# Optimization experiments

Measured on AMD Instinct MI355X. Metric: run time of the kernel, lower is better.

## Reference

```python
import jax, jax.numpy as jnp
import numpy as np


def _gru(x, w_ih, w_hh, b_ih, b_hh, reverse=False):
    # PyTorch GRU cell math. x: (N, T, Din) -> (N, T, Hh)
    N, T, _ = x.shape
    Hh = w_hh.shape[1]
    xp = jnp.einsum('ntd,gd->ntg', x, w_ih) + b_ih  # (N, T, 3*Hh), input gates precomputed

    def step(h, xp_t):
        gh = h @ w_hh.T + b_hh
        ir, iz, inn = jnp.split(xp_t, 3, axis=-1)
        hr, hz, hn = jnp.split(gh, 3, axis=-1)
        r = jax.nn.sigmoid(ir + hr)
        z = jax.nn.sigmoid(iz + hz)
        n = jnp.tanh(inn + r * hn)
        h_new = (1.0 - z) * n + z * h
        return h_new, h_new

    h0 = jnp.zeros((N, Hh), x.dtype)
    _, ys = jax.lax.scan(step, h0, jnp.swapaxes(xp, 0, 1), reverse=reverse)
    return jnp.swapaxes(ys, 0, 1)


def _bigru(x, pf, pb):
    return jnp.concatenate([_gru(x, *pf), _gru(x, *pb, reverse=True)], axis=-1)


def _attn(out, w, b, ctx):
    # out: (N, T, H). tanh(Linear) -> context dot -> softmax -> weighted sum
    u = jnp.tanh(jnp.einsum('nth,gh->ntg', out, w) + b)
    a = jax.nn.softmax(u @ ctx, axis=-1)  # (N, T)
    return jnp.einsum('nt,nth->nh', a, out)


def setup_inputs() -> dict:
    key = jax.random.key(0)
    H, Hh = 512, 256
    S, B, Nsent = 2048, 16, 16
    L = S // Nsent
    ks = jax.random.split(key, 32)

    def p(k, shape):
        return jax.random.normal(k, shape, jnp.float32) * 0.05

    starts = jnp.arange(Nsent, dtype=jnp.int32) * L
    spans = jnp.stack([starts, starts + L], axis=-1)  # (Nsent, 2)
    spans = jnp.broadcast_to(spans, (B, Nsent, 2))

    inp = {
        'token_feats': jax.random.normal(ks[0], (S, B, H), jnp.float32),
        'sentence_spans': spans,
        # word BiGRU params (forward / backward directions)
        'w_wih_f': p(ks[1], (3 * Hh, H)), 'w_whh_f': p(ks[2], (3 * Hh, Hh)),
        'w_bih_f': p(ks[3], (3 * Hh,)), 'w_bhh_f': p(ks[4], (3 * Hh,)),
        'w_wih_b': p(ks[5], (3 * Hh, H)), 'w_whh_b': p(ks[6], (3 * Hh, Hh)),
        'w_bih_b': p(ks[7], (3 * Hh,)), 'w_bhh_b': p(ks[8], (3 * Hh,)),
        # sentence BiGRU params
        's_wih_f': p(ks[9], (3 * Hh, H)), 's_whh_f': p(ks[10], (3 * Hh, Hh)),
        's_bih_f': p(ks[11], (3 * Hh,)), 's_bhh_f': p(ks[12], (3 * Hh,)),
        's_wih_b': p(ks[13], (3 * Hh, H)), 's_whh_b': p(ks[14], (3 * Hh, Hh)),
        's_bih_b': p(ks[15], (3 * Hh,)), 's_bhh_b': p(ks[16], (3 * Hh,)),
        # attention params
        'w_attn_w': p(ks[17], (H, H)), 'w_attn_b': p(ks[18], (H,)),
        'w_ctx': jax.random.normal(ks[19], (H,), jnp.float32),
        's_attn_w': p(ks[20], (H, H)), 's_attn_b': p(ks[21], (H,)),
        's_ctx': jax.random.normal(ks[22], (H,), jnp.float32),
    }
    return inp


def reference(token_feats, sentence_spans,
              w_wih_f, w_whh_f, w_bih_f, w_bhh_f,
              w_wih_b, w_whh_b, w_bih_b, w_bhh_b,
              s_wih_f, s_whh_f, s_bih_f, s_bhh_f,
              s_wih_b, s_whh_b, s_bih_b, s_bhh_b,
              w_attn_w, w_attn_b, w_ctx,
              s_attn_w, s_attn_b, s_ctx):
    S, B, H = token_feats.shape
    Nsent = sentence_spans.shape[1]
    L = S // Nsent  # uniform spans: segment b,i = tokens [i*L, (i+1)*L)

    x = jnp.swapaxes(token_feats, 0, 1)  # (B, S, H)
    segs = x.reshape(B * Nsent, L, H)    # all sentences batched together

    # word-level BiGRU + word attention -> sentence vectors
    out_w = _bigru(segs, (w_wih_f, w_whh_f, w_bih_f, w_bhh_f),
                   (w_wih_b, w_whh_b, w_bih_b, w_bhh_b))  # (B*Nsent, L, H)
    sent_vecs = _attn(out_w, w_attn_w, w_attn_b, w_ctx).reshape(B, Nsent, H)

    # sentence-level BiGRU + sentence attention (no padding: all masks true)
    out_s = _bigru(sent_vecs, (s_wih_f, s_whh_f, s_bih_f, s_bhh_f),
                   (s_wih_b, s_whh_b, s_bih_b, s_bhh_b))  # (B, Nsent, H)
    Yh = _attn(out_s, s_attn_w, s_attn_b, s_ctx)  # (B, H)
    return Yh
```

## Files before the change

### kernel.cpp

```cpp
#include <hip/hip_runtime.h>
#include <stdint.h>


using uint32  = unsigned int;
using bf16x8  = __attribute__((ext_vector_type(8))) __bf16;
using floatx4 = __attribute__((ext_vector_type(4))) float;

__device__ __forceinline__ float b2f(unsigned short u) {
    union { uint32 i; float f; } v; v.i = ((uint32)u) << 16; return v.f;
}
__device__ __forceinline__ unsigned short f2b(float f) {
    union { float f; uint32 i; } v; v.f = f;
    uint32 r = v.i + 0x7fffu + ((v.i >> 16) & 1u);
    return (unsigned short)(r >> 16);
}
__device__ __forceinline__ float sigmoidf_(float x) { return 1.f / (1.f + __expf(-x)); }
__device__ __forceinline__ float tanhf_(float x) {
    x = fminf(15.f, fmaxf(-15.f, x));
    float e = __expf(2.f * x);
    return (e - 1.f) / (e + 1.f);
}

__device__ __forceinline__ void gl16(const unsigned short* g, unsigned short* l) {
    __builtin_amdgcn_global_load_lds(
        (const __attribute__((address_space(1))) uint32*)g,
        (__attribute__((address_space(3))) uint32*)l, 16, 0, 0);
}

#define O_XPC     0L
#define O_OWHI    50331648L
#define O_OWLO    83886080L
#define O_STATE   117440512L
#define O_SCW     117964800L
#define O_W0HI    118095872L
#define O_W0LO    118882304L
#define O_W1HI    119668736L
#define O_W1LO    120455168L
#define O_WAHI    121241600L
#define O_WALO    121765888L
#define O_S0HI    122290176L
#define O_S0LO    123076608L
#define O_S1HI    123863040L
#define O_S1LO    124649472L
#define O_SAHI    125435904L
#define O_SALO    125960192L
#define O_HW0     126484480L
#define O_HW1     126877696L
#define O_HS0     127270912L
#define O_HS1     127664128L
#define O_SENTHI  128057344L
#define O_SENTLO  128319488L
#define O_XPS     128581632L
#define O_SSTATE  130154496L
#define O_OSHI    130187264L
#define O_OSLO    130449408L
#define O_SCS     130711552L
#define O_TKWH    130712576L
#define O_TKWL    147489792L

__global__ __launch_bounds__(256)
void cvt_hilo6(const float* __restrict__ s0, const float* __restrict__ s1,
               const float* __restrict__ s2, const float* __restrict__ s3,
               const float* __restrict__ s4, const float* __restrict__ s5,
               char* __restrict__ ws)
{
    const int b = blockIdx.x;
    const float* src; unsigned short *hi, *lo; int base;
    if (b < 192)      { src = s0; hi = (unsigned short*)(ws + O_W0HI); lo = (unsigned short*)(ws + O_W0LO); base = b; }
    else if (b < 384) { src = s1; hi = (unsigned short*)(ws + O_W1HI); lo = (unsigned short*)(ws + O_W1LO); base = b - 192; }
    else if (b < 576) { src = s2; hi = (unsigned short*)(ws + O_S0HI); lo = (unsigned short*)(ws + O_S0LO); base = b - 384; }
    else if (b < 768) { src = s3; hi = (unsigned short*)(ws + O_S1HI); lo = (unsigned short*)(ws + O_S1LO); base = b - 576; }
    else if (b < 896) { src = s4; hi = (unsigned short*)(ws + O_WAHI); lo = (unsigned short*)(ws + O_WALO); base = b - 768; }
    else              { src = s5; hi = (unsigned short*)(ws + O_SAHI); lo = (unsigned short*)(ws + O_SALO); base = b - 896; }
    const int idx = (base * 256 + threadIdx.x) * 8;
    float f[8];
    *reinterpret_cast<float4*>(&f[0]) = *reinterpret_cast<const float4*>(src + idx);
    *reinterpret_cast<float4*>(&f[4]) = *reinterpret_cast<const float4*>(src + idx + 4);
    unsigned short h[8], l[8];
    #pragma unroll
    for (int j = 0; j < 8; ++j) {
        h[j] = f2b(f[j]);
        l[j] = f2b(f[j] - b2f(h[j]));
    }
    *reinterpret_cast<uint4*>(hi + idx) = *reinterpret_cast<const uint4*>(h);
    *reinterpret_cast<uint4*>(lo + idx) = *reinterpret_cast<const uint4*>(l);
}

__global__ __launch_bounds__(256)
void cvt_b4(const float* __restrict__ s0, const float* __restrict__ s1,
            const float* __restrict__ s2, const float* __restrict__ s3,
            char* __restrict__ ws)
{
    const int b = blockIdx.x;
    const float* src; unsigned short* dst; int base;
    if (b < 96)       { src = s0; dst = (unsigned short*)(ws + O_HW0); base = b; }
    else if (b < 192) { src = s1; dst = (unsigned short*)(ws + O_HW1); base = b - 96; }
    else if (b < 288) { src = s2; dst = (unsigned short*)(ws + O_HS0); base = b - 192; }
    else              { src = s3; dst = (unsigned short*)(ws + O_HS1); base = b - 288; }
    const int idx = (base * 256 + threadIdx.x) * 8;
    float f[8];
    *reinterpret_cast<float4*>(&f[0]) = *reinterpret_cast<const float4*>(src + idx);
    *reinterpret_cast<float4*>(&f[4]) = *reinterpret_cast<const float4*>(src + idx + 4);
    unsigned short o[8];
    #pragma unroll
    for (int j = 0; j < 8; ++j) o[j] = f2b(f[j]);
    *reinterpret_cast<uint4*>(dst + idx) = *reinterpret_cast<const uint4*>(o);
}

__global__ __launch_bounds__(256)
void cvt_tokwin(const float* __restrict__ tok, unsigned short* __restrict__ whi,
                unsigned short* __restrict__ wlo, int c32)
{
    const int u = blockIdx.x * 256 + threadIdx.x;
    const int h8 = u & 63;
    const int rest = u >> 6;
    const int w = rest & 63, seq = rest >> 6;
    const int sent = seq & 15, b = seq >> 4;
    const int t = (w < 32) ? (c32 + w) : (96 - c32 + (w - 32));
    const long src = ((long)(sent * 128 + t) * 16 + b) * 512 + h8 * 8;
    float f[8];
    *reinterpret_cast<float4*>(&f[0]) = *reinterpret_cast<const float4*>(tok + src);
    *reinterpret_cast<float4*>(&f[4]) = *reinterpret_cast<const float4*>(tok + src + 4);
    unsigned short h[8], l[8];
    #pragma unroll
    for (int j = 0; j < 8; ++j) {
        h[j] = f2b(f[j]);
        l[j] = f2b(f[j] - b2f(h[j]));
    }
    const long dst = (long)rest * 512 + h8 * 8;
    *reinterpret_cast<uint4*>(whi + dst) = *reinterpret_cast<const uint4*>(h);
    *reinterpret_cast<uint4*>(wlo + dst) = *reinterpret_cast<const uint4*>(l);
}

template<int AMODE>
__device__ __forceinline__ long amap(int m, int t0, int sgn) {
    if (AMODE == 1) {
        const int sq = m >> 5, tl = m & 31;
        return (long)(sq * 64 + t0 + sgn * tl) * 512;
    } else if (AMODE == 3) {
        const int n = m >> 4, tl = m & 15;
        return (long)(n * 16 + t0 + sgn * tl) * 512;
    }
    return (long)m * 512;
}

template<int AMODE, int OUT>
__global__ __launch_bounds__(256)
void gemm_g(const unsigned short* __restrict__ Ahi, const unsigned short* __restrict__ Alo,
            const unsigned short* __restrict__ Wh0, const unsigned short* __restrict__ Wl0,
            const unsigned short* __restrict__ Wh1, const unsigned short* __restrict__ Wl1,
            const float* __restrict__ b0, const float* __restrict__ b1,
            float* __restrict__ C, int ldC, long c1off,
            float* __restrict__ score, const float* __restrict__ ctx,
            int t00, int t01, int nbyHalf)
{
    __shared__ __align__(16) unsigned short smem[16384];
    unsigned short* Ahs = smem;
    unsigned short* Als = smem + 4096;
    unsigned short* Whs = smem + 8192;
    unsigned short* Wls = smem + 12288;

    int bx = blockIdx.x, by = blockIdx.y;
    {
        const int nbx = gridDim.x, nby = gridDim.y;
        if ((nby & 7) == 0) {
            const int l = by * nbx + bx;
            const int xcd = l & 7;
            const int s = l >> 3;
            bx = s % nbx;
            by = xcd * (nby >> 3) + s / nbx;
        }
    }

    const int tid  = threadIdx.x;
    const int lane = tid & 63;
    const int wave = tid >> 6;
    const int wm = wave >> 1, wn = wave & 1;
    const int n_base = bx * 128;
    const int q = lane >> 4;
    const int r = lane & 15;

    const unsigned short* Whi = Wh0;
    const unsigned short* Wlo = Wl0;
    const float* bias = b0;
    float* Cb = C;
    int t0 = t00, sgn = 1, m_base;
    if (nbyHalf > 0 && by >= nbyHalf) {
        Whi = Wh1; Wlo = Wl1; bias = b1; Cb = C + c1off;
        t0 = t01; sgn = -1;
        m_base = (by - nbyHalf) * 128;
    } else {
        m_base = by * 128;
    }

    long aoff[2], woff[2];
    #pragma unroll
    for (int i = 0; i < 2; ++i) {
        const int s = tid + 256 * i;
        const int R = s >> 2, kg = s & 3;
        const int kq = (kg - (R >> 1)) & 3;
        aoff[i] = amap<AMODE>(m_base + R, t0, sgn) + kq * 8;
        woff[i] = (long)(n_base + R) * 512 + kq * 8;
    }

    floatx4 acc[4][4];
    #pragma unroll
    for (int mt = 0; mt < 4; ++mt)
        #pragma unroll
        for (int nt = 0; nt < 4; ++nt) acc[mt][nt] = (floatx4){0.f, 0.f, 0.f, 0.f};

    for (int k0 = 0; k0 < 512; k0 += 32) {
        #pragma unroll
        for (int i = 0; i < 2; ++i) {
            const int ld = tid * 8 + i * 2048;
            gl16(Ahi + aoff[i] + k0, Ahs + ld);
            gl16(Alo + aoff[i] + k0, Als + ld);
            gl16(Whi + woff[i] + k0, Whs + ld);
            gl16(Wlo + woff[i] + k0, Wls + ld);
        }
        __syncthreads();

        bf16x8 ah[4], al[4];
        #pragma unroll
        for (int mt = 0; mt < 4; ++mt) {
            const int R = wm * 64 + mt * 16 + r;
            const int s = R * 4 + ((q + (R >> 1)) & 3);
            ah[mt] = *reinterpret_cast<const bf16x8*>(Ahs + s * 8);
            al[mt] = *reinterpret_cast<const bf16x8*>(Als + s * 8);
        }
        #pragma unroll
        for (int nt = 0; nt < 4; ++nt) {
            const int Rn = wn * 64 + nt * 16 + r;
            const int s = Rn * 4 + ((q + (Rn >> 1)) & 3);
            bf16x8 wh = *reinterpret_cast<const bf16x8*>(Whs + s * 8);
            bf16x8 wl = *reinterpret_cast<const bf16x8*>(Wls + s * 8);
            #pragma unroll
            for (int mt = 0; mt < 4; ++mt) {
                acc[mt][nt] = __builtin_amdgcn_mfma_f32_16x16x32_bf16(ah[mt], wh, acc[mt][nt], 0, 0, 0);
                acc[mt][nt] = __builtin_amdgcn_mfma_f32_16x16x32_bf16(ah[mt], wl, acc[mt][nt], 0, 0, 0);
                acc[mt][nt] = __builtin_amdgcn_mfma_f32_16x16x32_bf16(al[mt], wh, acc[mt][nt], 0, 0, 0);
            }
        }
        __syncthreads();
    }

    if (OUT == 0) {
        #pragma unroll
        for (int nt = 0; nt < 4; ++nt) {
            const int n = n_base + wn * 64 + nt * 16 + r;
            const float bs = bias[n];
            #pragma unroll
            for (int mt = 0; mt < 4; ++mt) {
                const int m = m_base + wm * 64 + mt * 16 + q * 4;
                #pragma unroll
                for (int e = 0; e < 4; ++e)
                    Cb[(long)(m + e) * ldC + n] = acc[mt][nt][e] + bs;
            }
        }
    } else {
        #pragma unroll
        for (int mt = 0; mt < 4; ++mt) {
            float p[4] = {0.f, 0.f, 0.f, 0.f};
            #pragma unroll
            for (int nt = 0; nt < 4; ++nt) {
                const int n = n_base + wn * 64 + nt * 16 + r;
                const float cx = ctx[n];
                const float bs = bias[n];
                #pragma unroll
                for (int e = 0; e < 4; ++e)
                    p[e] += cx * tanhf_(acc[mt][nt][e] + bs);
            }
            #pragma unroll
            for (int mk = 1; mk < 16; mk <<= 1) {
                #pragma unroll
                for (int e = 0; e < 4; ++e) p[e] += __shfl_xor(p[e], mk, 64);
            }
            if (r == 0) {
                const int m = m_base + wm * 64 + mt * 16 + q * 4;
                #pragma unroll
                for (int e = 0; e < 4; ++e)
                    atomicAdd(&score[m + e], p[e]);
            }
        }
    }
}

__global__ __launch_bounds__(512, 2)
void gru2(const float* __restrict__ xp,
          const unsigned short* __restrict__ Wf,
          const unsigned short* __restrict__ Wb,
          const float* __restrict__ bhf, const float* __restrict__ bhb,
          float* __restrict__ state,
          unsigned short* __restrict__ ohi, unsigned short* __restrict__ olo,
          int steps, int t0f, int t0b, int groups, int Tout)
{
    __shared__ float pre[768 * 5];
    __shared__ unsigned short Bf[8 * 64 * 8];

    const int tid  = threadIdx.x;
    const int lane = tid & 63;
    const int w    = tid >> 6;
    const int dir  = blockIdx.x / groups;
    const int g    = blockIdx.x % groups;
    const int nseq = groups * 2;
    const unsigned short* W = dir ? Wb : Wf;
    const float* bh = dir ? bhb : bhf;
    const int t0  = dir ? t0b : t0f;
    const int sgn = dir ? -1 : 1;

    const int s = tid >> 8;
    const int j = tid & 255;
    const float bhr = bh[j], bhz = bh[j + 256], bhn = bh[j + 512];

    bf16x8 wf[6][8];
    {
        const int r0 = w * 96 + (lane & 15);
        const int kf = (lane >> 4) * 8;
        #pragma unroll
        for (int mt = 0; mt < 6; ++mt)
            #pragma unroll
            for (int kk = 0; kk < 8; ++kk)
                wf[mt][kk] = *reinterpret_cast<const bf16x8*>(
                    W + (long)(r0 + mt * 16) * 256 + kk * 32 + kf);
    }

    #pragma unroll
    for (int i = 0; i < 4; ++i)
        reinterpret_cast<uint32*>(Bf)[tid * 4 + i] = 0;

    float h = state[((long)dir * nseq + g * 2 + s) * 256 + j];
    const int posHi = ((j >> 5) * 64 + ((j >> 3) & 3) * 16 + s) * 8 + (j & 7);
    const int posLo = ((j >> 5) * 64 + ((j >> 3) & 3) * 16 + 2 + s) * 8 + (j & 7);
    {
        const unsigned short hb = f2b(h);
        Bf[posHi] = hb;
        Bf[posLo] = f2b(h - b2f(hb));
    }
    __syncthreads();

    const float* xbase = xp + (long)dir * nseq * steps * 768
                       + (long)(g * 2 + s) * steps * 768;
    const int q = lane >> 4, r = lane & 15;

    for (int st = 0; st < steps; ++st) {
        const int t = t0 + sgn * st;

        const float* xb = xbase + (long)st * 768;
        const float xr = xb[j];
        const float xz = xb[256 + j];
        const float xn = xb[512 + j];

        floatx4 acc[6];
        #pragma unroll
        for (int mt = 0; mt < 6; ++mt) acc[mt] = (floatx4){0.f, 0.f, 0.f, 0.f};
        #pragma unroll
        for (int kk = 0; kk < 8; ++kk) {
            bf16x8 bv = *reinterpret_cast<const bf16x8*>(Bf + (kk * 64 + lane) * 8);
            #pragma unroll
            for (int mt = 0; mt < 6; ++mt)
                acc[mt] = __builtin_amdgcn_mfma_f32_16x16x32_bf16(wf[mt][kk], bv, acc[mt], 0, 0, 0);
        }
        if (r < 4) {
            #pragma unroll
            for (int mt = 0; mt < 6; ++mt) {
                const int row = w * 96 + mt * 16 + q * 4;
                #pragma unroll
                for (int e = 0; e < 4; ++e)
                    pre[(row + e) * 5 + r] = acc[mt][e];
            }
        }
        __syncthreads();

        {
            const float pr = pre[j * 5 + s]         + pre[j * 5 + 2 + s];
            const float pz = pre[(j + 256) * 5 + s] + pre[(j + 256) * 5 + 2 + s];
            const float pn = pre[(j + 512) * 5 + s] + pre[(j + 512) * 5 + 2 + s];
            const float rg = sigmoidf_(xr + pr + bhr);
            const float zg = sigmoidf_(xz + pz + bhz);
            const float nn = tanhf_(xn + rg * (pn + bhn));
            h = (1.f - zg) * nn + zg * h;
            const unsigned short hb = f2b(h);
            const unsigned short lb = f2b(h - b2f(hb));
            Bf[posHi] = hb;
            Bf[posLo] = lb;
            const long orow = ((long)(g * 2 + s) * Tout + t) * 512 + dir * 256 + j;
            ohi[orow] = hb;
            olo[orow] = lb;
        }
        __syncthreads();
    }

    state[((long)dir * nseq + g * 2 + s) * 256 + j] = h;
}

template<int MODE>
__global__ __launch_bounds__(256)
void attn_wsum(const float* __restrict__ score,
               const unsigned short* __restrict__ fhi,
               const unsigned short* __restrict__ flo,
               void* __restrict__ o1, void* __restrict__ o2, int T)
{
    const int n = blockIdx.x;
    const int tid = threadIdx.x;
    __shared__ float a[128];
    if (tid < T) a[tid] = score[n * T + tid];
    __syncthreads();
    float mx = -1e30f;
    for (int t = 0; t < T; ++t) mx = fmaxf(mx, a[t]);
    float sm = 0.f;
    for (int t = 0; t < T; ++t) sm += __expf(a[t] - mx);
    const float inv = 1.f / sm;
    float acc0 = 0.f, acc1 = 0.f;
    for (int t = 0; t < T; ++t) {
        const float w = __expf(a[t] - mx) * inv;
        const long base = ((long)n * T + t) * 512;
        acc0 += w * (b2f(fhi[base + tid])       + b2f(flo[base + tid]));
        acc1 += w * (b2f(fhi[base + tid + 256]) + b2f(flo[base + tid + 256]));
    }
    if (MODE == 1) {
        float* o = (float*)o1;
        o[n * 512 + tid] = acc0;
        o[n * 512 + tid + 256] = acc1;
    } else {
        unsigned short* oh = (unsigned short*)o1;
        unsigned short* ol = (unsigned short*)o2;
        const unsigned short h0 = f2b(acc0), h1 = f2b(acc1);
        oh[n * 512 + tid]       = h0;  ol[n * 512 + tid]       = f2b(acc0 - b2f(h0));
        oh[n * 512 + tid + 256] = h1;  ol[n * 512 + tid + 256] = f2b(acc1 - b2f(h1));
    }
}

extern "C" void kernel_launch(void* const* d_in, const int* in_sizes, int n_in,
                              void* d_out, int out_size, void* d_ws, size_t ws_size,
                              hipStream_t stream) {
    const float* tok      = (const float*)d_in[0];
    const float* w_wih_f  = (const float*)d_in[2];
    const float* w_whh_f  = (const float*)d_in[3];
    const float* w_bih_f  = (const float*)d_in[4];
    const float* w_bhh_f  = (const float*)d_in[5];
    const float* w_wih_b  = (const float*)d_in[6];
    const float* w_whh_b  = (const float*)d_in[7];
    const float* w_bih_b  = (const float*)d_in[8];
    const float* w_bhh_b  = (const float*)d_in[9];
    const float* s_wih_f  = (const float*)d_in[10];
    const float* s_whh_f  = (const float*)d_in[11];
    const float* s_bih_f  = (const float*)d_in[12];
    const float* s_bhh_f  = (const float*)d_in[13];
    const float* s_wih_b  = (const float*)d_in[14];
    const float* s_whh_b  = (const float*)d_in[15];
    const float* s_bih_b  = (const float*)d_in[16];
    const float* s_bhh_b  = (const float*)d_in[17];
    const float* w_attn_b = (const float*)d_in[19];
    const float* w_ctx    = (const float*)d_in[20];
    const float* s_attn_b = (const float*)d_in[22];
    const float* s_ctx    = (const float*)d_in[23];

    char* ws = (char*)d_ws;
    float*          xpc   = (float*)(ws + O_XPC);
    unsigned short* owhi  = (unsigned short*)(ws + O_OWHI);
    unsigned short* owlo  = (unsigned short*)(ws + O_OWLO);
    float*          state = (float*)(ws + O_STATE);
    float*          score_w = (float*)(ws + O_SCW);
    unsigned short* W0HI  = (unsigned short*)(ws + O_W0HI);
    unsigned short* W0LO  = (unsigned short*)(ws + O_W0LO);
    unsigned short* W1HI  = (unsigned short*)(ws + O_W1HI);
    unsigned short* W1LO  = (unsigned short*)(ws + O_W1LO);
    unsigned short* WAHI  = (unsigned short*)(ws + O_WAHI);
    unsigned short* WALO  = (unsigned short*)(ws + O_WALO);
    unsigned short* S0HI  = (unsigned short*)(ws + O_S0HI);
    unsigned short* S0LO  = (unsigned short*)(ws + O_S0LO);
    unsigned short* S1HI  = (unsigned short*)(ws + O_S1HI);
    unsigned short* S1LO  = (unsigned short*)(ws + O_S1LO);
    unsigned short* SAHI  = (unsigned short*)(ws + O_SAHI);
    unsigned short* SALO  = (unsigned short*)(ws + O_SALO);
    unsigned short* HW0   = (unsigned short*)(ws + O_HW0);
    unsigned short* HW1   = (unsigned short*)(ws + O_HW1);
    unsigned short* HS0   = (unsigned short*)(ws + O_HS0);
    unsigned short* HS1   = (unsigned short*)(ws + O_HS1);
    unsigned short* senthi = (unsigned short*)(ws + O_SENTHI);
    unsigned short* sentlo = (unsigned short*)(ws + O_SENTLO);
    float*          xp_s  = (float*)(ws + O_XPS);
    float*          sstate = (float*)(ws + O_SSTATE);
    unsigned short* oshi  = (unsigned short*)(ws + O_OSHI);
    unsigned short* oslo  = (unsigned short*)(ws + O_OSLO);
    float*          score_s = (float*)(ws + O_SCS);
    unsigned short* tkwh  = (unsigned short*)(ws + O_TKWH);
    unsigned short* tkwl  = (unsigned short*)(ws + O_TKWL);

    const dim3 blk(256);

    hipMemsetAsync(ws + O_STATE,  0, 524288, stream);
    hipMemsetAsync(ws + O_SSTATE, 0, 32768, stream);
    hipMemsetAsync(ws + O_SCW,    0, 131072, stream);
    hipMemsetAsync(ws + O_SCS,    0, 1024, stream);

    cvt_hilo6<<<dim3(1024), blk, 0, stream>>>(w_wih_f, w_wih_b, s_wih_f, s_wih_b,
                                              (const float*)d_in[18], (const float*)d_in[21], ws);
    cvt_b4<<<dim3(384), blk, 0, stream>>>(w_whh_f, w_whh_b, s_whh_f, s_whh_b, ws);

    const long XDW = 256L * 32 * 768;
    for (int c = 0; c < 4; ++c) {
        cvt_tokwin<<<dim3(4096), blk, 0, stream>>>(tok, tkwh, tkwl, 32 * c);
        gemm_g<1, 0><<<dim3(6, 128), blk, 0, stream>>>(
            tkwh, tkwl, W0HI, W0LO, W1HI, W1LO, w_bih_f, w_bih_b,
            xpc, 768, XDW, nullptr, nullptr, 0, 63, 64);
        gru2<<<dim3(256), dim3(512), 0, stream>>>(
            xpc, HW0, HW1, w_bhh_f, w_bhh_b, state, owhi, owlo,
            32, 32 * c, 127 - 32 * c, 128, 128);
    }

    gemm_g<2, 1><<<dim3(4, 256), blk, 0, stream>>>(
        owhi, owlo, WAHI, WALO, WAHI, WALO, w_attn_b, w_attn_b,
        nullptr, 0, 0, score_w, w_ctx, 0, 0, 0);
    attn_wsum<0><<<dim3(256), blk, 0, stream>>>(score_w, owhi, owlo, senthi, sentlo, 128);

    const long XDS = 16L * 16 * 768;
    gemm_g<3, 0><<<dim3(6, 4), blk, 0, stream>>>(
        senthi, sentlo, S0HI, S0LO, S1HI, S1LO, s_bih_f, s_bih_b,
        xp_s, 768, XDS, nullptr, nullptr, 0, 15, 2);

    gru2<<<dim3(16), dim3(512), 0, stream>>>(
        xp_s, HS0, HS1, s_bhh_f, s_bhh_b, sstate, oshi, oslo,
        16, 0, 15, 8, 16);

    gemm_g<2, 1><<<dim3(4, 2), blk, 0, stream>>>(
        oshi, oslo, SAHI, SALO, SAHI, SALO, s_attn_b, s_attn_b,
        nullptr, 0, 0, score_s, s_ctx, 0, 0, 0);
    attn_wsum<1><<<dim3(16), blk, 0, stream>>>(score_s, oshi, oslo, d_out, nullptr, 16);
}
```

Measured before the change: 785.5 us.

## Triple-buffer GEMM k-loop, convert tokens once, prefetch GRU inputs, precompute softmax exps

The split-bf16 GEMM is restructured into 48 stages that each load one hi/lo operand pair into a 3-deep LDS ring buffer. A stage is prefetched two steps ahead, and a raw waitcnt plus barrier replaces __syncthreads. Token conversion to hi/lo bf16 is hoisted out of the per-chunk loop into one full conversion, which doubles the token workspace. The GRU kernel prefetches the next timestep's input projections and uses lighter barriers. attn_wsum is templated on T and computes the exponentials once into shared memory. Together these aim to hide global-load latency and cut repeated conversion and exp work, at the cost of more LDS and a larger workspace.

Result: faster. 724.0 us (-7.8%).

```diff
diff --git a/kernel.cpp b/kernel.cpp
--- a/kernel.cpp
+++ b/kernel.cpp
@@ -56,7 +56,7 @@
 #define O_OSLO    130449408L
 #define O_SCS     130711552L
 #define O_TKWH    130712576L
-#define O_TKWL    147489792L
+#define O_TKWL    164267008L
 
 __global__ __launch_bounds__(256)
 void cvt_hilo6(const float* __restrict__ s0, const float* __restrict__ s1,
@@ -108,15 +108,14 @@
 }
 
 __global__ __launch_bounds__(256)
-void cvt_tokwin(const float* __restrict__ tok, unsigned short* __restrict__ whi,
-                unsigned short* __restrict__ wlo, int c32)
+void cvt_tokfull(const float* __restrict__ tok, unsigned short* __restrict__ whi,
+                 unsigned short* __restrict__ wlo)
 {
     const int u = blockIdx.x * 256 + threadIdx.x;
     const int h8 = u & 63;
     const int rest = u >> 6;
-    const int w = rest & 63, seq = rest >> 6;
+    const int t = rest & 127, seq = rest >> 7;
     const int sent = seq & 15, b = seq >> 4;
-    const int t = (w < 32) ? (c32 + w) : (96 - c32 + (w - 32));
     const long src = ((long)(sent * 128 + t) * 16 + b) * 512 + h8 * 8;
     float f[8];
     *reinterpret_cast<float4*>(&f[0]) = *reinterpret_cast<const float4*>(tok + src);
@@ -136,7 +135,7 @@
 __device__ __forceinline__ long amap(int m, int t0, int sgn) {
     if (AMODE == 1) {
         const int sq = m >> 5, tl = m & 31;
-        return (long)(sq * 64 + t0 + sgn * tl) * 512;
+        return (long)(sq * 128 + t0 + sgn * tl) * 512;
     } else if (AMODE == 3) {
         const int n = m >> 4, tl = m & 15;
         return (long)(n * 16 + t0 + sgn * tl) * 512;
@@ -146,7 +145,7 @@
 
 template<int AMODE, int OUT>
 __global__ __launch_bounds__(256)
-void gemm_g(const unsigned short* __restrict__ Ahi, const unsigned short* __restrict__ Alo,
+void gemm_p(const unsigned short* __restrict__ Ahi, const unsigned short* __restrict__ Alo,
             const unsigned short* __restrict__ Wh0, const unsigned short* __restrict__ Wl0,
             const unsigned short* __restrict__ Wh1, const unsigned short* __restrict__ Wl1,
             const float* __restrict__ b0, const float* __restrict__ b1,
@@ -154,11 +153,7 @@
             float* __restrict__ score, const float* __restrict__ ctx,
             int t00, int t01, int nbyHalf)
 {
-    __shared__ __align__(16) unsigned short smem[16384];
-    unsigned short* Ahs = smem;
-    unsigned short* Als = smem + 4096;
-    unsigned short* Whs = smem + 8192;
-    unsigned short* Wls = smem + 12288;
+    __shared__ __align__(16) unsigned short smem[3 * 8192];
 
     int bx = blockIdx.x, by = blockIdx.y;
     {
@@ -209,40 +204,49 @@
         #pragma unroll
         for (int nt = 0; nt < 4; ++nt) acc[mt][nt] = (floatx4){0.f, 0.f, 0.f, 0.f};
 
-    for (int k0 = 0; k0 < 512; k0 += 32) {
+    auto stage = [&](int ts) {
+        const int buf = ts % 3;
+        const int kr  = ts >> 4;
+        const int kk  = (ts & 15) * 32;
+        const unsigned short* Ap = (kr == 2) ? Alo : Ahi;
+        const unsigned short* Wp = (kr == 1) ? Wlo : Whi;
+        unsigned short* LA = smem + buf * 8192;
+        unsigned short* LW = LA + 4096;
         #pragma unroll
         for (int i = 0; i < 2; ++i) {
-            const int ld = tid * 8 + i * 2048;
-            gl16(Ahi + aoff[i] + k0, Ahs + ld);
-            gl16(Alo + aoff[i] + k0, Als + ld);
-            gl16(Whi + woff[i] + k0, Whs + ld);
-            gl16(Wlo + woff[i] + k0, Wls + ld);
-        }
-        __syncthreads();
-
-        bf16x8 ah[4], al[4];
+            gl16(Ap + aoff[i] + kk, LA + (tid + 256 * i) * 8);
+            gl16(Wp + woff[i] + kk, LW + (tid + 256 * i) * 8);
+        }
+    };
+
+    stage(0);
+    stage(1);
+    for (int t = 0; t < 48; ++t) {
+        stage(t + 2 < 48 ? t + 2 : 47);
+        asm volatile("s_waitcnt vmcnt(8)\n\ts_barrier" ::: "memory");
+
+        const unsigned short* LA = smem + (t % 3) * 8192;
+        const unsigned short* LW = LA + 4096;
+        bf16x8 ah[4], wh[4];
         #pragma unroll
         for (int mt = 0; mt < 4; ++mt) {
             const int R = wm * 64 + mt * 16 + r;
-            const int s = R * 4 + ((q + (R >> 1)) & 3);
-            ah[mt] = *reinterpret_cast<const bf16x8*>(Ahs + s * 8);
-            al[mt] = *reinterpret_cast<const bf16x8*>(Als + s * 8);
+            ah[mt] = *reinterpret_cast<const bf16x8*>(LA + (R * 4 + ((q + (R >> 1)) & 3)) * 8);
         }
         #pragma unroll
         for (int nt = 0; nt < 4; ++nt) {
             const int Rn = wn * 64 + nt * 16 + r;
-            const int s = Rn * 4 + ((q + (Rn >> 1)) & 3);
-            bf16x8 wh = *reinterpret_cast<const bf16x8*>(Whs + s * 8);
-            bf16x8 wl = *reinterpret_cast<const bf16x8*>(Wls + s * 8);
-            #pragma unroll
-            for (int mt = 0; mt < 4; ++mt) {
-                acc[mt][nt] = __builtin_amdgcn_mfma_f32_16x16x32_bf16(ah[mt], wh, acc[mt][nt], 0, 0, 0);
-                acc[mt][nt] = __builtin_amdgcn_mfma_f32_16x16x32_bf16(ah[mt], wl, acc[mt][nt], 0, 0, 0);
-                acc[mt][nt] = __builtin_amdgcn_mfma_f32_16x16x32_bf16(al[mt], wh, acc[mt][nt], 0, 0, 0);
-            }
-        }
-        __syncthreads();
-    }
+            wh[nt] = *reinterpret_cast<const bf16x8*>(LW + (Rn * 4 + ((q + (Rn >> 1)) & 3)) * 8);
+        }
+        #pragma unroll
+        for (int nt = 0; nt < 4; ++nt)
+            #pragma unroll
+            for (int mt = 0; mt < 4; ++mt)
+                acc[mt][nt] = __builtin_amdgcn_mfma_f32_16x16x32_bf16(ah[mt], wh[nt], acc[mt][nt], 0, 0, 0);
+
+        asm volatile("s_waitcnt lgkmcnt(0)\n\ts_barrier" ::: "memory");
+    }
+    asm volatile("s_waitcnt vmcnt(0)" ::: "memory");
 
     if (OUT == 0) {
         #pragma unroll
@@ -336,19 +340,22 @@
         Bf[posHi] = hb;
         Bf[posLo] = f2b(h - b2f(hb));
     }
-    __syncthreads();
+    asm volatile("s_waitcnt lgkmcnt(0)\n\ts_barrier" ::: "memory");
 
     const float* xbase = xp + (long)dir * nseq * steps * 768
                        + (long)(g * 2 + s) * steps * 768;
     const int q = lane >> 4, r = lane & 15;
 
+    float xr = xbase[j], xz = xbase[256 + j], xn = xbase[512 + j];
+
     for (int st = 0; st < steps; ++st) {
         const int t = t0 + sgn * st;
 
-        const float* xb = xbase + (long)st * 768;
-        const float xr = xb[j];
-        const float xz = xb[256 + j];
-        const float xn = xb[512 + j];
+        const int sn = (st + 1 < steps) ? st + 1 : st;
+        const float* xb = xbase + (long)sn * 768;
+        const float nxr = xb[j];
+        const float nxz = xb[256 + j];
+        const float nxn = xb[512 + j];
 
         floatx4 acc[6];
         #pragma unroll
@@ -369,7 +376,7 @@
                     pre[(row + e) * 5 + r] = acc[mt][e];
             }
         }
-        __syncthreads();
+        asm volatile("s_waitcnt lgkmcnt(0)\n\ts_barrier" ::: "memory");
 
         {
             const float pr = pre[j * 5 + s]         + pre[j * 5 + 2 + s];
@@ -387,32 +394,39 @@
             ohi[orow] = hb;
             olo[orow] = lb;
         }
-        __syncthreads();
+        xr = nxr; xz = nxz; xn = nxn;
+        asm volatile("s_waitcnt lgkmcnt(0)\n\ts_barrier" ::: "memory");
     }
 
     state[((long)dir * nseq + g * 2 + s) * 256 + j] = h;
 }
 
-template<int MODE>
+template<int MODE, int T>
 __global__ __launch_bounds__(256)
 void attn_wsum(const float* __restrict__ score,
                const unsigned short* __restrict__ fhi,
                const unsigned short* __restrict__ flo,
-               void* __restrict__ o1, void* __restrict__ o2, int T)
+               void* __restrict__ o1, void* __restrict__ o2)
 {
     const int n = blockIdx.x;
     const int tid = threadIdx.x;
-    __shared__ float a[128];
+    __shared__ float a[T];
+    __shared__ float e[T];
     if (tid < T) a[tid] = score[n * T + tid];
     __syncthreads();
     float mx = -1e30f;
+    #pragma unroll
     for (int t = 0; t < T; ++t) mx = fmaxf(mx, a[t]);
+    if (tid < T) e[tid] = __expf(a[tid] - mx);
+    __syncthreads();
     float sm = 0.f;
-    for (int t = 0; t < T; ++t) sm += __expf(a[t] - mx);
+    #pragma unroll
+    for (int t = 0; t < T; ++t) sm += e[t];
     const float inv = 1.f / sm;
     float acc0 = 0.f, acc1 = 0.f;
+    #pragma unroll 8
     for (int t = 0; t < T; ++t) {
-        const float w = __expf(a[t] - mx) * inv;
+        const float w = e[t] * inv;
         const long base = ((long)n * T + t) * 512;
         acc0 += w * (b2f(fhi[base + tid])       + b2f(flo[base + tid]));
         acc1 += w * (b2f(fhi[base + tid + 256]) + b2f(flo[base + tid + 256]));
@@ -497,25 +511,25 @@
     cvt_hilo6<<<dim3(1024), blk, 0, stream>>>(w_wih_f, w_wih_b, s_wih_f, s_wih_b,
                                               (const float*)d_in[18], (const float*)d_in[21], ws);
     cvt_b4<<<dim3(384), blk, 0, stream>>>(w_whh_f, w_whh_b, s_whh_f, s_whh_b, ws);
+    cvt_tokfull<<<dim3(8192), blk, 0, stream>>>(tok, tkwh, tkwl);
 
     const long XDW = 256L * 32 * 768;
     for (int c = 0; c < 4; ++c) {
-        cvt_tokwin<<<dim3(4096), blk, 0, stream>>>(tok, tkwh, tkwl, 32 * c);
-        gemm_g<1, 0><<<dim3(6, 128), blk, 0, stream>>>(
+        gemm_p<1, 0><<<dim3(6, 128), blk, 0, stream>>>(
             tkwh, tkwl, W0HI, W0LO, W1HI, W1LO, w_bih_f, w_bih_b,
-            xpc, 768, XDW, nullptr, nullptr, 0, 63, 64);
+            xpc, 768, XDW, nullptr, nullptr, 32 * c, 127 - 32 * c, 64);
         gru2<<<dim3(256), dim3(512), 0, stream>>>(
             xpc, HW0, HW1, w_bhh_f, w_bhh_b, state, owhi, owlo,
             32, 32 * c, 127 - 32 * c, 128, 128);
     }
 
-    gemm_g<2, 1><<<dim3(4, 256), blk, 0, stream>>>(
+    gemm_p<2, 1><<<dim3(4, 256), blk, 0, stream>>>(
         owhi, owlo, WAHI, WALO, WAHI, WALO, w_attn_b, w_attn_b,
         nullptr, 0, 0, score_w, w_ctx, 0, 0, 0);
-    attn_wsum<0><<<dim3(256), blk, 0, stream>>>(score_w, owhi, owlo, senthi, sentlo, 128);
+    attn_wsum<0, 128><<<dim3(256), blk, 0, stream>>>(score_w, owhi, owlo, senthi, sentlo);
 
     const long XDS = 16L * 16 * 768;
-    gemm_g<3, 0><<<dim3(6, 4), blk, 0, stream>>>(
+    gemm_p<3, 0><<<dim3(6, 4), blk, 0, stream>>>(
         senthi, sentlo, S0HI, S0LO, S1HI, S1LO, s_bih_f, s_bih_b,
         xp_s, 768, XDS, nullptr, nullptr, 0, 15, 2);
 
@@ -523,8 +537,8 @@
         xp_s, HS0, HS1, s_bhh_f, s_bhh_b, sstate, oshi, oslo,
         16, 0, 15, 8, 16);
 
-    gemm_g<2, 1><<<dim3(4, 2), blk, 0, stream>>>(
+    gemm_p<2, 1><<<dim3(4, 2), blk, 0, stream>>>(
         oshi, oslo, SAHI, SALO, SAHI, SALO, s_attn_b, s_attn_b,
         nullptr, 0, 0, score_s, s_ctx, 0, 0, 0);
-    attn_wsum<1><<<dim3(16), blk, 0, stream>>>(score_s, oshi, oslo, d_out, nullptr, 16);
-}
+    attn_wsum<1, 16><<<dim3(16), blk, 0, stream>>>(score_s, oshi, oslo, d_out, nullptr);
+}
```
